# Optimization experiments

Hardware: AMD Instinct MI355X
Metric: run time of the kernel (lower is better)

The kernel has to match this reference:

```python
import jax, jax.numpy as jnp
import numpy as np

B, C, H, W = 4, 512, 64, 64
RED = 8
D = max(1, C // RED)  # inter_channels = 64
BN_EPS = 1e-5


def conv1x1(x, w, b):
    # x: [B,Cin,H,W], w: [Cout,Cin], b: [Cout]
    return jnp.einsum('oc,bchw->bohw', w, x) + b[None, :, None, None]


def setup_inputs() -> dict:
    key = jax.random.key(0)
    ks = jax.random.split(key, 12)
    s = 0.02
    return {
        'x': jax.random.normal(ks[0], (B, C, H, W), jnp.float32),
        'theta_w': jax.random.normal(ks[1], (D, C), jnp.float32) * s,
        'theta_b': jax.random.normal(ks[2], (D,), jnp.float32) * s,
        'phi_w': jax.random.normal(ks[3], (D, C), jnp.float32) * s,
        'phi_b': jax.random.normal(ks[4], (D,), jnp.float32) * s,
        'g_w': jax.random.normal(ks[5], (D, C), jnp.float32) * s,
        'g_b': jax.random.normal(ks[6], (D,), jnp.float32) * s,
        'out_w': jax.random.normal(ks[7], (C, D), jnp.float32) * s,
        'out_b': jax.random.normal(ks[8], (C,), jnp.float32) * s,
        'bn_gamma': jnp.ones((C,), jnp.float32),
        'bn_beta': jnp.zeros((C,), jnp.float32),
        'scale': jax.random.normal(ks[9], (1,), jnp.float32) * 0.1,
    }


def reference(x, theta_w, theta_b, phi_w, phi_b, g_w, g_b,
              out_w, out_b, bn_gamma, bn_beta, scale):
    b, c, h, w = x.shape
    n = h * w
    theta = conv1x1(x, theta_w, theta_b).reshape(b, D, n)  # [B,D,N]
    phi = conv1x1(x, phi_w, phi_b).reshape(b, D, n)        # [B,D,N]
    g = conv1x1(x, g_w, g_b).reshape(b, D, n)              # [B,D,N]
    # attention[b,i,j] = sum_d theta[b,d,i] * phi[b,d,j] (unscaled)
    attn = jax.nn.softmax(jnp.einsum('bdi,bdj->bij', theta, phi), axis=-1)
    # y[b,d,i] = sum_j g[b,d,j] * attn[b,i,j]
    y = jnp.einsum('bdj,bij->bdi', g, attn).reshape(b, D, h, w)
    y = conv1x1(y, out_w, out_b)  # [B,C,H,W]
    # BatchNorm2d, training-mode batch statistics over (B,H,W)
    mean = jnp.mean(y, axis=(0, 2, 3), keepdims=True)
    var = jnp.var(y, axis=(0, 2, 3), keepdims=True)
    y = (y - mean) * jax.lax.rsqrt(var + BN_EPS)
    y = y * bn_gamma[None, :, None, None] + bn_beta[None, :, None, None]
    return x + scale.reshape(()) * y
```

## Files before the change

kernel.cpp:

```cpp
#include <hip/hip_runtime.h>
#include <hip/hip_bf16.h>
#include <math.h>

#define NPIX 4096
#define CIN  512
#define DD   64
#define BB   4
#define NCHUNK 8

using f32x4  = __attribute__((ext_vector_type(4))) float;
using bf16x8 = __attribute__((ext_vector_type(8))) short;
using u16x4  = __attribute__((ext_vector_type(4))) unsigned short;
using u32x2  = __attribute__((ext_vector_type(2))) unsigned int;

__device__ __forceinline__ unsigned short f2bf(float f){
    union { __hip_bfloat16 h; unsigned short u; } v;
    v.h = __float2bfloat16(f);
    return v.u;
}

__device__ __forceinline__ float bf2f(unsigned short u){
    union { unsigned u; float f; } v; v.u = ((unsigned)u) << 16; return v.f;
}

__device__ __forceinline__ unsigned pk2(float a, float b){
    union { __hip_bfloat162 h; unsigned u; } v;
    v.h = __float22bfloat162_rn(make_float2(a, b));
    return v.u;
}

__device__ __forceinline__ bf16x8 cvt8(float4 a, float4 b){
    union { unsigned u[4]; bf16x8 v; } r;
    r.u[0] = pk2(a.x, a.y); r.u[1] = pk2(a.z, a.w);
    r.u[2] = pk2(b.x, b.y); r.u[3] = pk2(b.z, b.w);
    return r.v;
}

__global__ __launch_bounds__(256, 4) void k1_qkv(
    const float* __restrict__ x,
    const float* __restrict__ tw, const float* __restrict__ tbv,
    const float* __restrict__ pw, const float* __restrict__ pbv,
    const float* __restrict__ gw, const float* __restrict__ gbv,
    unsigned short* __restrict__ thetaT, unsigned short* __restrict__ phiT,
    unsigned short* __restrict__ g_dn)
{
    const int n0 = blockIdx.x * 64;
    const int kt = blockIdx.y;
    const int b  = blockIdx.z;
    const int tid = threadIdx.x;
    const float* W  = (kt==0) ? tw  : (kt==1) ? pw  : gw;
    const float* Bv = (kt==0) ? tbv : (kt==1) ? pbv : gbv;
    const float wsc = (kt==0) ? 1.4426950408889634f : 1.0f;

    const int wq   = tid >> 6;
    const int lane = tid & 63;
    const int lr   = lane & 15;
    const int lg   = lane >> 4;

    __shared__ __align__(16) unsigned short T[64*72];
    __shared__ __align__(16) short Wt[64*72];
    __shared__ __align__(16) short Xt[64*72];

    f32x4 acc[4];
    #pragma unroll
    for (int jt=0;jt<4;++jt) acc[jt] = (f32x4){0.f,0.f,0.f,0.f};

    const int srow = tid >> 2;
    const int skq  = (tid & 3) * 16;

    for (int k0 = 0; k0 < CIN; k0 += 64) {
        __syncthreads();
        {
            const float* wp = W + (size_t)srow*CIN + k0 + skq;
            float4 w0 = *reinterpret_cast<const float4*>(wp);
            float4 w1 = *reinterpret_cast<const float4*>(wp + 4);
            float4 w2 = *reinterpret_cast<const float4*>(wp + 8);
            float4 w3 = *reinterpret_cast<const float4*>(wp + 12);
            w0.x*=wsc; w0.y*=wsc; w0.z*=wsc; w0.w*=wsc;
            w1.x*=wsc; w1.y*=wsc; w1.z*=wsc; w1.w*=wsc;
            w2.x*=wsc; w2.y*=wsc; w2.z*=wsc; w2.w*=wsc;
            w3.x*=wsc; w3.y*=wsc; w3.z*=wsc; w3.w*=wsc;
            *reinterpret_cast<bf16x8*>(&Wt[srow*72 + skq])     = cvt8(w0, w1);
            *reinterpret_cast<bf16x8*>(&Wt[srow*72 + skq + 8]) = cvt8(w2, w3);
            const float* xp = x + ((size_t)b*CIN + k0 + srow)*NPIX + n0 + skq;
            float4 a0 = *reinterpret_cast<const float4*>(xp);
            float4 a1 = *reinterpret_cast<const float4*>(xp + 4);
            float4 a2 = *reinterpret_cast<const float4*>(xp + 8);
            float4 a3 = *reinterpret_cast<const float4*>(xp + 12);
            *reinterpret_cast<bf16x8*>(&T[srow*72 + skq])     = cvt8(a0, a1);
            *reinterpret_cast<bf16x8*>(&T[srow*72 + skq + 8]) = cvt8(a2, a3);
        }
        __syncthreads();
        {
            unsigned short v[16];
            #pragma unroll
            for (int i=0;i<16;++i) v[i] = T[(skq+i)*72 + srow];
            *reinterpret_cast<bf16x8*>(&Xt[srow*72 + skq])     = *reinterpret_cast<bf16x8*>(&v[0]);
            *reinterpret_cast<bf16x8*>(&Xt[srow*72 + skq + 8]) = *reinterpret_cast<bf16x8*>(&v[8]);
        }
        __syncthreads();

        __builtin_amdgcn_s_setprio(1);
        #pragma unroll
        for (int dc=0;dc<2;++dc){
            bf16x8 af = *reinterpret_cast<const bf16x8*>(&Wt[(wq*16+lr)*72 + dc*32 + lg*8]);
            #pragma unroll
            for (int jt=0;jt<4;++jt){
                bf16x8 bf = *reinterpret_cast<const bf16x8*>(&Xt[(jt*16+lr)*72 + dc*32 + lg*8]);
                acc[jt] = __builtin_amdgcn_mfma_f32_16x16x32_bf16(af, bf, acc[jt], 0,0,0);
            }
        }
        __builtin_amdgcn_s_setprio(0);
    }

    const int mb = wq*16 + lg*4;
    float bv[4];
    #pragma unroll
    for (int r=0;r<4;++r) bv[r] = Bv[mb+r] * wsc;

    if (kt < 2){
        unsigned short* dst = (kt==0) ? thetaT : phiT;
        #pragma unroll
        for (int jt=0;jt<4;++jt){
            union { unsigned u[2]; u16x4 v; } o;
            o.u[0] = pk2(acc[jt][0]+bv[0], acc[jt][1]+bv[1]);
            o.u[1] = pk2(acc[jt][2]+bv[2], acc[jt][3]+bv[3]);
            *reinterpret_cast<u16x4*>(&dst[((size_t)b*NPIX + n0 + jt*16+lr)*DD + mb]) = o.v;
        }
    } else {
        #pragma unroll
        for (int jt=0;jt<4;++jt)
            #pragma unroll
            for (int r=0;r<4;++r)
                g_dn[((size_t)b*DD + mb+r)*NPIX + n0 + jt*16+lr] = f2bf(acc[jt][r]+bv[r]);
    }
}

__global__ __launch_bounds__(256, 4) void k2_attn(
    const unsigned short* __restrict__ thetaT,
    const unsigned short* __restrict__ phiT,
    const unsigned short* __restrict__ g_dn,
    unsigned short* __restrict__ pY, float* __restrict__ pL)
{
    const int i0 = blockIdx.x * 128;
    const int ch = blockIdx.y;
    const int b  = blockIdx.z;
    const int tid  = threadIdx.x;
    const int wq   = tid >> 6;
    const int lane = tid & 63;
    const int lr   = lane & 15;
    const int lg   = lane >> 4;

    __shared__ __align__(16) short Kt[64*72];
    __shared__ __align__(16) short Gt[64*72];
    __shared__ __align__(16) short Pb[4*32*72];
    short* Pw = &Pb[wq*32*72];

    bf16x8 qf0[2], qf1[2];
    {
        const unsigned short* qp0 = thetaT + ((size_t)b*NPIX + i0 + wq*16 + lr)*DD + lg*8;
        qf0[0] = *reinterpret_cast<const bf16x8*>(qp0);
        qf0[1] = *reinterpret_cast<const bf16x8*>(qp0 + 32);
        const unsigned short* qp1 = qp0 + (size_t)64*DD;
        qf1[0] = *reinterpret_cast<const bf16x8*>(qp1);
        qf1[1] = *reinterpret_cast<const bf16x8*>(qp1 + 32);
    }
    const bf16x8 onesf = { (short)0x3F80,(short)0x3F80,(short)0x3F80,(short)0x3F80,
                           (short)0x3F80,(short)0x3F80,(short)0x3F80,(short)0x3F80 };

    f32x4 yacc0[4], yacc1[4], lacc0, lacc1;
    #pragma unroll
    for (int dt=0;dt<4;++dt){
        yacc0[dt] = (f32x4){0.f,0.f,0.f,0.f};
        yacc1[dt] = (f32x4){0.f,0.f,0.f,0.f};
    }
    lacc0 = (f32x4){0.f,0.f,0.f,0.f};
    lacc1 = (f32x4){0.f,0.f,0.f,0.f};

    const unsigned short* phb = phiT + (size_t)b*NPIX*DD;
    const unsigned short* gb  = g_dn + (size_t)b*DD*NPIX;

    const int jbeg = ch * (NPIX / NCHUNK);
    const int jend = jbeg + (NPIX / NCHUNK);

    const int srow = tid >> 3;
    const int scb  = (tid & 7) * 8;

    for (int j0 = jbeg; j0 < jend; j0 += 64) {
        __syncthreads();
        *reinterpret_cast<float4*>(&Kt[srow*72 + scb]) =
            *reinterpret_cast<const float4*>(&phb[(size_t)(j0+srow)*DD + scb]);
        *reinterpret_cast<float4*>(&Kt[(srow+32)*72 + scb]) =
            *reinterpret_cast<const float4*>(&phb[(size_t)(j0+srow+32)*DD + scb]);
        *reinterpret_cast<float4*>(&Gt[srow*72 + scb]) =
            *reinterpret_cast<const float4*>(&gb[(size_t)srow*NPIX + j0 + scb]);
        *reinterpret_cast<float4*>(&Gt[(srow+32)*72 + scb]) =
            *reinterpret_cast<const float4*>(&gb[(size_t)(srow+32)*NPIX + j0 + scb]);
        __syncthreads();

        f32x4 s0[4], s1[4];
        #pragma unroll
        for (int jt=0;jt<4;++jt){
            s0[jt] = (f32x4){0.f,0.f,0.f,0.f};
            s1[jt] = (f32x4){0.f,0.f,0.f,0.f};
        }
        __builtin_amdgcn_s_setprio(1);
        #pragma unroll
        for (int dc=0;dc<2;++dc){
            #pragma unroll
            for (int jt=0;jt<4;++jt){
                bf16x8 bf = *reinterpret_cast<const bf16x8*>(&Kt[(jt*16+lr)*72 + dc*32 + lg*8]);
                s0[jt] = __builtin_amdgcn_mfma_f32_16x16x32_bf16(bf, qf0[dc], s0[jt], 0,0,0);
                s1[jt] = __builtin_amdgcn_mfma_f32_16x16x32_bf16(bf, qf1[dc], s1[jt], 0,0,0);
            }
        }
        __builtin_amdgcn_s_setprio(0);

        #pragma unroll
        for (int jt=0;jt<4;++jt){
            u32x2 w0, w1;
            w0.x = pk2(exp2f(s0[jt][0]), exp2f(s0[jt][1]));
            w0.y = pk2(exp2f(s0[jt][2]), exp2f(s0[jt][3]));
            *reinterpret_cast<u32x2*>(&Pw[lr*72      + jt*16 + lg*4]) = w0;
            w1.x = pk2(exp2f(s1[jt][0]), exp2f(s1[jt][1]));
            w1.y = pk2(exp2f(s1[jt][2]), exp2f(s1[jt][3]));
            *reinterpret_cast<u32x2*>(&Pw[(16+lr)*72 + jt*16 + lg*4]) = w1;
        }

        __builtin_amdgcn_s_setprio(1);
        #pragma unroll
        for (int jc=0;jc<2;++jc){
            bf16x8 af0 = *reinterpret_cast<const bf16x8*>(&Pw[lr*72      + jc*32 + lg*8]);
            bf16x8 af1 = *reinterpret_cast<const bf16x8*>(&Pw[(16+lr)*72 + jc*32 + lg*8]);
            #pragma unroll
            for (int dt=0;dt<4;++dt){
                bf16x8 gf = *reinterpret_cast<const bf16x8*>(&Gt[(dt*16+lr)*72 + jc*32 + lg*8]);
                yacc0[dt] = __builtin_amdgcn_mfma_f32_16x16x32_bf16(af0, gf, yacc0[dt], 0,0,0);
                yacc1[dt] = __builtin_amdgcn_mfma_f32_16x16x32_bf16(af1, gf, yacc1[dt], 0,0,0);
            }
            lacc0 = __builtin_amdgcn_mfma_f32_16x16x32_bf16(af0, onesf, lacc0, 0,0,0);
            lacc1 = __builtin_amdgcn_mfma_f32_16x16x32_bf16(af1, onesf, lacc1, 0,0,0);
        }
        __builtin_amdgcn_s_setprio(0);
    }

    {
        unsigned short* py0 = pY + (((size_t)b*NCHUNK + ch)*NPIX + i0 + wq*16)*DD;
        unsigned short* py1 = py0 + (size_t)64*DD;
        #pragma unroll
        for (int r=0;r<4;++r)
            #pragma unroll
            for (int dt=0;dt<4;++dt){
                py0[(size_t)(lg*4+r)*DD + dt*16 + lr] = f2bf(yacc0[dt][r]);
                py1[(size_t)(lg*4+r)*DD + dt*16 + lr] = f2bf(yacc1[dt][r]);
            }
        if (lr == 0){
            const size_t base = ((size_t)b*NCHUNK + ch)*NPIX + i0 + wq*16;
            #pragma unroll
            for (int r=0;r<4;++r){
                pL[base + lg*4+r]      = lacc0[r];
                pL[base + 64 + lg*4+r] = lacc1[r];
            }
        }
    }
}

__global__ __launch_bounds__(256) void k3_out(
    const unsigned short* __restrict__ pY, const float* __restrict__ pL,
    const float* __restrict__ ow, const float* __restrict__ ob,
    unsigned short* __restrict__ y2b,
    float* __restrict__ psum, float* __restrict__ qsum)
{
    const int n0 = blockIdx.x * 64;
    const int c0 = blockIdx.y * 64;
    const int b  = blockIdx.z;
    const int tid = threadIdx.x;
    const int wq   = tid >> 6;
    const int lane = tid & 63;
    const int lr   = lane & 15;
    const int lg   = lane >> 4;

    __shared__ __align__(16) short Ot[64*72];
    __shared__ __align__(16) short Yt[64*72];

    {
        const int srow = tid >> 2, skq = (tid & 3) * 16;
        const float* wp = ow + (size_t)(c0+srow)*DD + skq;
        float4 w0 = *reinterpret_cast<const float4*>(wp);
        float4 w1 = *reinterpret_cast<const float4*>(wp + 4);
        float4 w2 = *reinterpret_cast<const float4*>(wp + 8);
        float4 w3 = *reinterpret_cast<const float4*>(wp + 12);
        *reinterpret_cast<bf16x8*>(&Ot[srow*72 + skq])     = cvt8(w0, w1);
        *reinterpret_cast<bf16x8*>(&Ot[srow*72 + skq + 8]) = cvt8(w2, w3);

        float ya[16];
        #pragma unroll
        for (int i=0;i<16;++i) ya[i] = 0.f;
        float lsum = 0.f;
        #pragma unroll
        for (int c=0;c<NCHUNK;++c){
            const unsigned short* yp =
                pY + (((size_t)b*NCHUNK + c)*NPIX + n0 + srow)*DD + skq;
            bf16x8 v0 = *reinterpret_cast<const bf16x8*>(yp);
            bf16x8 v1 = *reinterpret_cast<const bf16x8*>(yp + 8);
            #pragma unroll
            for (int i=0;i<8;++i){
                ya[i]   += bf2f((unsigned short)v0[i]);
                ya[8+i] += bf2f((unsigned short)v1[i]);
            }
            lsum += pL[((size_t)b*NCHUNK + c)*NPIX + n0 + srow];
        }
        const float inv = 1.f / lsum;
        union { unsigned u[8]; bf16x8 v[2]; } o;
        #pragma unroll
        for (int i=0;i<8;++i) o.u[i] = pk2(ya[2*i]*inv, ya[2*i+1]*inv);
        *reinterpret_cast<bf16x8*>(&Yt[srow*72 + skq])     = o.v[0];
        *reinterpret_cast<bf16x8*>(&Yt[srow*72 + skq + 8]) = o.v[1];
    }
    __syncthreads();

    f32x4 acc[4];
    #pragma unroll
    for (int jt=0;jt<4;++jt) acc[jt] = (f32x4){0.f,0.f,0.f,0.f};
    #pragma unroll
    for (int dc=0;dc<2;++dc){
        bf16x8 af = *reinterpret_cast<const bf16x8*>(&Ot[(wq*16+lr)*72 + dc*32 + lg*8]);
        #pragma unroll
        for (int jt=0;jt<4;++jt){
            bf16x8 bf = *reinterpret_cast<const bf16x8*>(&Yt[(jt*16+lr)*72 + dc*32 + lg*8]);
            acc[jt] = __builtin_amdgcn_mfma_f32_16x16x32_bf16(af, bf, acc[jt], 0,0,0);
        }
    }

    const int cb = c0 + wq*16 + lg*4;
    float bv[4];
    #pragma unroll
    for (int r=0;r<4;++r) bv[r] = ob[cb+r];

    float sr[4] = {0,0,0,0}, qr[4] = {0,0,0,0};
    #pragma unroll
    for (int jt=0;jt<4;++jt)
        #pragma unroll
        for (int r=0;r<4;++r){
            float v = acc[jt][r] + bv[r];
            y2b[((size_t)b*CIN + cb+r)*NPIX + n0 + jt*16+lr] = f2bf(v);
            sr[r] += v; qr[r] += v*v;
        }
    #pragma unroll
    for (int off=1; off<16; off<<=1)
        #pragma unroll
        for (int r=0;r<4;++r){
            sr[r] += __shfl_xor(sr[r], off);
            qr[r] += __shfl_xor(qr[r], off);
        }
    if (lr == 0){
        const int slot = b*64 + blockIdx.x;
        #pragma unroll
        for (int r=0;r<4;++r){
            psum[(size_t)(cb+r)*256 + slot] = sr[r];
            qsum[(size_t)(cb+r)*256 + slot] = qr[r];
        }
    }
}

__global__ __launch_bounds__(256) void k3b_stats(
    const float* __restrict__ psum, const float* __restrict__ qsum,
    float* __restrict__ meanA, float* __restrict__ invA)
{
    const int c = blockIdx.x;
    const int tid = threadIdx.x;
    float s = psum[(size_t)c*256 + tid];
    float q = qsum[(size_t)c*256 + tid];
    __shared__ float rs[256], rq[256];
    rs[tid]=s; rq[tid]=q; __syncthreads();
    for (int off=128; off; off>>=1){
        if (tid<off){ rs[tid]+=rs[tid+off]; rq[tid]+=rq[tid+off]; }
        __syncthreads();
    }
    if (tid==0){
        const float n = (float)(BB*NPIX);
        float mm = rs[0] / n;
        float v = rq[0] / n - mm*mm;
        meanA[c]=mm; invA[c]=rsqrtf(v + 1e-5f);
    }
}

__global__ __launch_bounds__(256) void k4_final(
    const float* __restrict__ x, const unsigned short* __restrict__ y2b,
    const float* __restrict__ meanA, const float* __restrict__ invA,
    const float* __restrict__ gamma, const float* __restrict__ beta,
    const float* __restrict__ scale, float* __restrict__ out)
{
    const float sc = scale[0];
    const int total4 = BB*CIN*NPIX/4;
    for (int i4 = blockIdx.x*blockDim.x + threadIdx.x; i4 < total4;
         i4 += gridDim.x*blockDim.x){
        int c = (i4 >> 10) & (CIN-1);
        float4 xv = reinterpret_cast<const float4*>(x)[i4];
        ushort4 yv = reinterpret_cast<const ushort4*>(y2b)[i4];
        float mm = meanA[c], iv = invA[c], g = gamma[c], bt = beta[c];
        float4 o;
        o.x = xv.x + sc*(g*(bf2f(yv.x)-mm)*iv + bt);
        o.y = xv.y + sc*(g*(bf2f(yv.y)-mm)*iv + bt);
        o.z = xv.z + sc*(g*(bf2f(yv.z)-mm)*iv + bt);
        o.w = xv.w + sc*(g*(bf2f(yv.w)-mm)*iv + bt);
        reinterpret_cast<float4*>(out)[i4] = o;
    }
}

extern "C" void kernel_launch(void* const* d_in, const int* in_sizes, int n_in,
                              void* d_out, int out_size, void* d_ws, size_t ws_size,
                              hipStream_t stream)
{
    const float* x     = (const float*)d_in[0];
    const float* tw    = (const float*)d_in[1];
    const float* tbv   = (const float*)d_in[2];
    const float* pw    = (const float*)d_in[3];
    const float* pbv   = (const float*)d_in[4];
    const float* gw    = (const float*)d_in[5];
    const float* gbv   = (const float*)d_in[6];
    const float* ow    = (const float*)d_in[7];
    const float* ob    = (const float*)d_in[8];
    const float* gamma = (const float*)d_in[9];
    const float* beta  = (const float*)d_in[10];
    const float* scale = (const float*)d_in[11];
    float* out = (float*)d_out;

    char* wsb = (char*)d_ws;
    unsigned short* thetaT = (unsigned short*)(wsb);
    unsigned short* phiT   = (unsigned short*)(wsb + 2097152);
    unsigned short* g_dn   = (unsigned short*)(wsb + 4194304);
    float*          pL     = (float*)(wsb + 8388608);
    float*          psum   = (float*)(wsb + 8912896);
    float*          qsum   = (float*)(wsb + 9437184);
    float*          meanA  = (float*)(wsb + 9961472);
    float*          invA   = (float*)(wsb + 9963520);
    unsigned short* y2b    = (unsigned short*)(wsb + 16777216);

    unsigned short* pY = (unsigned short*)d_out;

    k1_qkv <<<dim3(64,3,4), 256, 0, stream>>>(x, tw, tbv, pw, pbv, gw, gbv,
                                              thetaT, phiT, g_dn);
    k2_attn<<<dim3(32,NCHUNK,4), 256, 0, stream>>>(thetaT, phiT, g_dn, pY, pL);
    k3_out <<<dim3(64,8,4), 256, 0, stream>>>(pY, pL, ow, ob, y2b, psum, qsum);
    k3b_stats<<<512, 256, 0, stream>>>(psum, qsum, meanA, invA);
    k4_final<<<2048, 256, 0, stream>>>(x, y2b, meanA, invA, gamma, beta, scale, out);
}
```

Baseline: 86.17 us.

## Double-buffer attention K/G tiles via direct global-to-LDS loads with XOR swizzle

Replaces the synchronous register-staged copies of the phi and g tiles in the attention kernel with global_load_lds DMA into a double-buffered LDS layout. The next tile is prefetched while the current one is being computed, and one barrier per iteration is dropped. An XOR swizzle replaces row padding to avoid LDS bank conflicts. This doubles LDS for K/G, which may reduce occupancy, and correctness depends on the async loads completing before the barrier.

```diff
diff --git a/kernel.cpp b/kernel.cpp
--- a/kernel.cpp
+++ b/kernel.cpp
@@ -34,6 +34,12 @@
     r.u[0] = pk2(a.x, a.y); r.u[1] = pk2(a.z, a.w);
     r.u[2] = pk2(b.x, b.y); r.u[3] = pk2(b.z, b.w);
     return r.v;
+}
+
+__device__ __forceinline__ void gload_lds16(const void* g, void* l){
+    __builtin_amdgcn_global_load_lds(
+        (const __attribute__((address_space(1))) unsigned int*)g,
+        (__attribute__((address_space(3))) unsigned int*)l, 16, 0, 0);
 }
 
 __global__ __launch_bounds__(256, 4) void k1_qkv(
@@ -151,10 +157,37 @@
     const int lr   = lane & 15;
     const int lg   = lane >> 4;
 
-    __shared__ __align__(16) short Kt[64*72];
-    __shared__ __align__(16) short Gt[64*72];
+    __shared__ __align__(16) short Kt[2*64*64];
+    __shared__ __align__(16) short Gt[2*64*64];
     __shared__ __align__(16) short Pb[4*32*72];
     short* Pw = &Pb[wq*32*72];
+    char*  KtB = (char*)Kt;
+    char*  GtB = (char*)Gt;
+
+    const unsigned short* phb = phiT + (size_t)b*NPIX*DD;
+    const unsigned short* gb  = g_dn + (size_t)b*DD*NPIX;
+
+    const int sseg  = wq & 1;
+    const int lrow  = lane >> 3;
+    const int lcolB = (lane & 7) << 4;
+    const int scolX = lcolB ^ (lrow << 4);
+
+    #define K2STAGE(BUF, J0) { \
+        if (wq < 2){ \
+            const char* gs = (const char*)phb + ((size_t)((J0) + sseg*32 + lrow))*128 + scolX; \
+            char* ls = KtB + (BUF)*8192 + sseg*4096; \
+            gload_lds16(gs,            ls); \
+            gload_lds16(gs +  8*128,   ls + 1024); \
+            gload_lds16(gs + 16*128,   ls + 2048); \
+            gload_lds16(gs + 24*128,   ls + 3072); \
+        } else { \
+            const char* gs = (const char*)gb + ((size_t)(sseg*32 + lrow))*8192 + (size_t)(J0)*2 + scolX; \
+            char* ls = GtB + (BUF)*8192 + sseg*4096; \
+            gload_lds16(gs,             ls); \
+            gload_lds16(gs +  8*8192,   ls + 1024); \
+            gload_lds16(gs + 16*8192,   ls + 2048); \
+            gload_lds16(gs + 24*8192,   ls + 3072); \
+        } }
 
     bf16x8 qf0[2], qf1[2];
     {
@@ -177,26 +210,20 @@
     lacc0 = (f32x4){0.f,0.f,0.f,0.f};
     lacc1 = (f32x4){0.f,0.f,0.f,0.f};
 
-    const unsigned short* phb = phiT + (size_t)b*NPIX*DD;
-    const unsigned short* gb  = g_dn + (size_t)b*DD*NPIX;
-
     const int jbeg = ch * (NPIX / NCHUNK);
     const int jend = jbeg + (NPIX / NCHUNK);
-
-    const int srow = tid >> 3;
-    const int scb  = (tid & 7) * 8;
-
+    const int swzK = (lr & 7) << 4;
+
+    K2STAGE(0, jbeg);
+    __syncthreads();
+
+    int cur = 0;
     for (int j0 = jbeg; j0 < jend; j0 += 64) {
-        __syncthreads();
-        *reinterpret_cast<float4*>(&Kt[srow*72 + scb]) =
-            *reinterpret_cast<const float4*>(&phb[(size_t)(j0+srow)*DD + scb]);
-        *reinterpret_cast<float4*>(&Kt[(srow+32)*72 + scb]) =
-            *reinterpret_cast<const float4*>(&phb[(size_t)(j0+srow+32)*DD + scb]);
-        *reinterpret_cast<float4*>(&Gt[srow*72 + scb]) =
-            *reinterpret_cast<const float4*>(&gb[(size_t)srow*NPIX + j0 + scb]);
-        *reinterpret_cast<float4*>(&Gt[(srow+32)*72 + scb]) =
-            *reinterpret_cast<const float4*>(&gb[(size_t)(srow+32)*NPIX + j0 + scb]);
-        __syncthreads();
+        const bool more = (j0 + 64 < jend);
+        if (more) K2STAGE(cur^1, j0 + 64);
+
+        const char* kc = KtB + cur*8192;
+        const char* gc = GtB + cur*8192;
 
         f32x4 s0[4], s1[4];
         #pragma unroll
@@ -209,7 +236,8 @@
         for (int dc=0;dc<2;++dc){
             #pragma unroll
             for (int jt=0;jt<4;++jt){
-                bf16x8 bf = *reinterpret_cast<const bf16x8*>(&Kt[(jt*16+lr)*72 + dc*32 + lg*8]);
+                bf16x8 bf = *reinterpret_cast<const bf16x8*>(
+                    kc + (jt*16+lr)*128 + ((dc*64 + lg*16) ^ swzK));
                 s0[jt] = __builtin_amdgcn_mfma_f32_16x16x32_bf16(bf, qf0[dc], s0[jt], 0,0,0);
                 s1[jt] = __builtin_amdgcn_mfma_f32_16x16x32_bf16(bf, qf1[dc], s1[jt], 0,0,0);
             }
@@ -234,7 +262,8 @@
             bf16x8 af1 = *reinterpret_cast<const bf16x8*>(&Pw[(16+lr)*72 + jc*32 + lg*8]);
             #pragma unroll
             for (int dt=0;dt<4;++dt){
-                bf16x8 gf = *reinterpret_cast<const bf16x8*>(&Gt[(dt*16+lr)*72 + jc*32 + lg*8]);
+                bf16x8 gf = *reinterpret_cast<const bf16x8*>(
+                    gc + (dt*16+lr)*128 + ((jc*64 + lg*16) ^ swzK));
                 yacc0[dt] = __builtin_amdgcn_mfma_f32_16x16x32_bf16(af0, gf, yacc0[dt], 0,0,0);
                 yacc1[dt] = __builtin_amdgcn_mfma_f32_16x16x32_bf16(af1, gf, yacc1[dt], 0,0,0);
             }
@@ -242,7 +271,13 @@
             lacc1 = __builtin_amdgcn_mfma_f32_16x16x32_bf16(af1, onesf, lacc1, 0,0,0);
         }
         __builtin_amdgcn_s_setprio(0);
-    }
+
+        if (more){
+            __syncthreads();
+            cur ^= 1;
+        }
+    }
+    #undef K2STAGE
 
     {
         unsigned short* py0 = pY + (((size_t)b*NCHUNK + ch)*NPIX + i0 + wq*16)*DD;
```

New measurement: 88.25 us. 1.02x slower.
